# Kernel tuning notes

Measured on AMD Instinct MI355X. Metric: run time of the kernel, lower is better.

Reference implementation:

```python
import jax, jax.numpy as jnp
import numpy as np

H = 50  # hidden size
I = 1   # input size


def setup_inputs() -> dict:
    key = jax.random.key(0)
    ks = jax.random.split(key, 7)
    B, T = 4096, 512
    s = 1.0 / np.sqrt(H)  # PyTorch default init scale
    x = jax.random.normal(ks[0], (B, T, I), dtype=jnp.float32)
    W_ih = jax.random.uniform(ks[1], (4 * H, I), jnp.float32, -s, s)
    W_hh = jax.random.uniform(ks[2], (4 * H, H), jnp.float32, -s, s)
    b_ih = jax.random.uniform(ks[3], (4 * H,), jnp.float32, -s, s)
    b_hh = jax.random.uniform(ks[4], (4 * H,), jnp.float32, -s, s)
    W_out = jax.random.uniform(ks[5], (1, H), jnp.float32, -s, s)
    b_out = jax.random.uniform(ks[6], (1,), jnp.float32, -s, s)
    return {"x": x, "W_ih": W_ih, "W_hh": W_hh, "b_ih": b_ih,
            "b_hh": b_hh, "W_out": W_out, "b_out": b_out}


def _lstm(x, W_ih, W_hh, b_ih, b_hh):
    # x: [B, T, I]; gate order in PyTorch: i, f, g, o
    B = x.shape[0]
    b = b_ih + b_hh
    # precompute input projection for all timesteps: [T, B, 4H]
    xg = jnp.einsum('bti,gi->tbg', x, W_ih) + b

    def step(carry, xg_t):
        h, c = carry
        gates = xg_t + h @ W_hh.T  # [B, 4H]
        i, f, g, o = jnp.split(gates, 4, axis=-1)
        c = jax.nn.sigmoid(f) * c + jax.nn.sigmoid(i) * jnp.tanh(g)
        h = jax.nn.sigmoid(o) * jnp.tanh(c)
        return (h, c), h

    h0 = jnp.zeros((B, H), x.dtype)
    c0 = jnp.zeros((B, H), x.dtype)
    _, hs = jax.lax.scan(step, (h0, c0), xg)  # hs: [T, B, H]
    return hs.transpose(1, 0, 2)  # [B, T, H]


def reference(x, W_ih, W_hh, b_ih, b_hh, W_out, b_out):
    h = _lstm(x, W_ih, W_hh, b_ih, b_hh)          # [B, T, H]
    return h @ W_out.T + b_out                     # [B, T, 1]
```

## Files before the change

### kernel.cpp

```cpp
#include <hip/hip_runtime.h>
#include <math.h>

#define HID 50
#define TT  512
#define BT  16
#define NTH 448
#define HS  72
#define L2E 1.44269504088896f
#define K2C 2.88539008177793f

typedef __attribute__((ext_vector_type(8))) short bf16x8;
typedef __attribute__((ext_vector_type(4))) float f32x4;

__device__ __forceinline__ unsigned short bf16_rtne(float f) {
    unsigned u = __float_as_uint(f);
    u = (u + 0x7FFFu + ((u >> 16) & 1u)) >> 16;
    return (unsigned short)u;
}
__device__ __forceinline__ float bf16_f32(unsigned short s) {
    return __uint_as_float(((unsigned)s) << 16);
}

__global__ __launch_bounds__(NTH, 1) void lstm_mfma19_kernel(
    const float* __restrict__ x,
    const float* __restrict__ W_ih,
    const float* __restrict__ W_hh,
    const float* __restrict__ b_ih,
    const float* __restrict__ b_hh,
    const float* __restrict__ W_out,
    const float* __restrict__ b_out,
    float* __restrict__ out)
{
    const int tid  = threadIdx.x;
    const int lane = tid & 63;
    const int wv   = tid >> 6;
    const int col  = lane & 15;
    const int quad = lane >> 4;

    __shared__ __align__(16) unsigned short Hh[2][BT][HS];

    for (int i = tid; i < 2 * BT * HS; i += NTH)
        (&Hh[0][0][0])[i] = 0;

    bf16x8 Ah[2][2];
    float cs0 = 0.f, cs1 = 0.f;
    const int uoa = wv * 8 + quad;
    const int uob = wv * 8 + 4 + quad;
    const int uom = (quad == 1) ? 48 : (quad == 2) ? 49 : (quad == 0) ? 55 : 56;
    const int s0 = (wv < 6) ? uoa : uom;
    const int s1 = (wv < 6) ? uob : 57;

    if (wv < 6) {
        #pragma unroll
        for (int i = 0; i < 2; ++i) {
            const int gh  = (wv * 2 + i) * 16 + col;
            const int u   = gh >> 2;
            const int ty  = gh & 3;
            const int og  = ty * HID + u;
            const float sc = (ty == 2) ? K2C : L2E;
            #pragma unroll
            for (int kk = 0; kk < 2; ++kk) {
                #pragma unroll
                for (int j = 0; j < 8; ++j) {
                    const int k = kk * 32 + quad * 8 + j;
                    float v = 0.f;
                    if (k < HID)      v = sc * W_hh[og * HID + k];
                    else if (k == 50) v = sc * W_ih[og];
                    else if (k == 51) v = sc * (b_ih[og] + b_hh[og]);
                    else if (k == 52) v = sc * W_ih[og];
                    else if (k == 53) {
                        const float sb = sc * (b_ih[og] + b_hh[og]);
                        v = sb - bf16_f32(bf16_rtne(sb));
                    } else if (k == 54) {
                        const float sw = sc * W_ih[og];
                        v = sw - bf16_f32(bf16_rtne(sw));
                    }
                    Ah[i][kk][j] = (short)bf16_rtne(v);
                }
            }
        }
    } else {
        #pragma unroll
        for (int kk = 0; kk < 2; ++kk) {
            #pragma unroll
            for (int j = 0; j < 8; ++j) {
                const int k = kk * 32 + quad * 8 + j;
                float v = 0.f;
                if (col < 2) {
                    if (k < HID) {
                        const float w = W_out[k];
                        v = (col == 0) ? w : w - bf16_f32(bf16_rtne(w));
                    }
                } else if (col >= 4 && col < 12) {
                    const int u  = (col < 8) ? 48 : 49;
                    const int ty = col & 3;
                    const int og = ty * HID + u;
                    const float sc = (ty == 2) ? K2C : L2E;
                    if (k < HID)      v = sc * W_hh[og * HID + k];
                    else if (k == 50) v = sc * W_ih[og];
                    else if (k == 51) v = sc * (b_ih[og] + b_hh[og]);
                    else if (k == 52) v = sc * W_ih[og];
                    else if (k == 53) {
                        const float sb = sc * (b_ih[og] + b_hh[og]);
                        v = sb - bf16_f32(bf16_rtne(sb));
                    } else if (k == 54) {
                        const float sw = sc * W_ih[og];
                        v = sw - bf16_f32(bf16_rtne(sw));
                    }
                }
                Ah[0][kk][j] = (short)bf16_rtne(v);
                Ah[1][kk][j] = 0;
            }
        }
    }
    const float bo = b_out[0];
    float* yout = out + (size_t)blockIdx.x * BT * TT + (size_t)col * TT;

    const float* xrow = x + (size_t)(blockIdx.x * BT + col) * TT;
    float xa = 0.f;
    if (wv == 6 && lane >= 48)
        xa = xrow[1];

    __syncthreads();

    if (tid < BT) {
        const float x0 = x[(size_t)(blockIdx.x * BT + tid) * TT];
        const unsigned short hx = bf16_rtne(x0);
        const unsigned short lx = bf16_rtne(x0 - bf16_f32(hx));
        unsigned* row32 = (unsigned*)&Hh[0][tid][0];
        row32[25] = (unsigned)hx | (0x3F80u << 16);
        row32[26] = (unsigned)lx | (0x3F80u << 16);
        Hh[0][tid][54] = hx;
    }
    __syncthreads();

    const unsigned short* rdA = &Hh[0][col][quad * 8];
    const unsigned short* rdB = &Hh[1][col][quad * 8];
    unsigned short* wrA0 = &Hh[1][col][s0];
    unsigned short* wrA1 = &Hh[1][col][s1];
    unsigned short* wrB0 = &Hh[0][col][s0];
    unsigned short* wrB1 = &Hh[0][col][s1];
    unsigned* xwA = (unsigned*)&Hh[1][col][0];
    unsigned* xwB = (unsigned*)&Hh[0][col][0];
    const f32x4 z = {0.f, 0.f, 0.f, 0.f};

#define GATES(ACC, CS, HOUT)                                                  \
    do {                                                                      \
        const float Ei = __builtin_amdgcn_exp2f(-(ACC).x);                    \
        const float Ef = __builtin_amdgcn_exp2f(-(ACC).y);                    \
        const float Eg = __builtin_amdgcn_exp2f((ACC).z);                     \
        const float Eo = __builtin_amdgcn_exp2f(-(ACC).w);                    \
        const float DIG = (1.f + Ei) * (1.f + Eg);                            \
        const float DF  = 1.f + Ef;                                           \
        const float t1  = fmaf(K2C, Eg, -K2C);                                \
        const float num = fmaf((CS), DIG, t1 * DF);                           \
        (CS) = num * __builtin_amdgcn_rcpf(DF * DIG);                         \
        const float Ec = __builtin_amdgcn_exp2f(CS);                          \
        (HOUT) = (Ec - 1.f) *                                                 \
                 __builtin_amdgcn_rcpf((1.f + Eo) * (1.f + Ec));              \
    } while (0)

#define LSTM_STEP(RD, WR0, WR1, XW, TI)                                       \
    do {                                                                      \
        const bf16x8 B0 = *(const bf16x8*)(RD);                               \
        const bf16x8 B1 = *(const bf16x8*)((RD) + 32);                        \
        if (wv < 6) {                                                         \
            f32x4 a0 = __builtin_amdgcn_mfma_f32_16x16x32_bf16(Ah[0][0], B0, z, 0, 0, 0); \
            f32x4 a1 = __builtin_amdgcn_mfma_f32_16x16x32_bf16(Ah[1][0], B0, z, 0, 0, 0); \
            a0 = __builtin_amdgcn_mfma_f32_16x16x32_bf16(Ah[0][1], B1, a0, 0, 0, 0); \
            a1 = __builtin_amdgcn_mfma_f32_16x16x32_bf16(Ah[1][1], B1, a1, 0, 0, 0); \
            float h0, h1;                                                     \
            GATES(a0, cs0, h0);                                               \
            GATES(a1, cs1, h1);                                               \
            unsigned hpk;                                                     \
            asm("v_cvt_pk_bf16_f32 %0, %1, %2" : "=v"(hpk) : "v"(h0), "v"(h1)); \
            *(WR0) = (unsigned short)(hpk & 0xFFFFu);                         \
            *(WR1) = (unsigned short)(hpk >> 16);                             \
        } else {                                                              \
            if (lane >= 48) {                                                 \
                const unsigned short hx = bf16_rtne(xa);                      \
                const unsigned short lx = bf16_rtne(xa - bf16_f32(hx));       \
                (XW)[25] = (unsigned)hx | (0x3F80u << 16);                    \
                (XW)[26] = (unsigned)lx | (0x3F80u << 16);                    \
                ((unsigned short*)(XW))[54] = hx;                             \
                xa = xrow[((TI) + 2 < TT) ? (TI) + 2 : TT - 1];               \
            }                                                                 \
            f32x4 a0 = __builtin_amdgcn_mfma_f32_16x16x32_bf16(Ah[0][0], B0, z, 0, 0, 0); \
            a0 = __builtin_amdgcn_mfma_f32_16x16x32_bf16(Ah[0][1], B1, a0, 0, 0, 0); \
            float h0;                                                         \
            GATES(a0, cs0, h0);                                               \
            unsigned hpk;                                                     \
            asm("v_cvt_pk_bf16_f32 %0, %1, %2" : "=v"(hpk) : "v"(h0), "v"(h0)); \
            *(WR0) = (unsigned short)(hpk & 0xFFFFu);                         \
            if (lane < 16 && (TI) > 0)                                        \
                yout[(TI) - 1] = a0.x + a0.y + bo;                            \
        }                                                                     \
    } while (0)

    for (int t = 0; t < TT; t += 2) {
        LSTM_STEP(rdA, wrA0, wrA1, xwA, t);
        asm volatile("s_waitcnt lgkmcnt(0)\n\ts_barrier" ::: "memory");
        LSTM_STEP(rdB, wrB0, wrB1, xwB, t + 1);
        asm volatile("s_waitcnt lgkmcnt(0)\n\ts_barrier" ::: "memory");
    }
#undef LSTM_STEP
#undef GATES

    if (wv == 6) {
        const bf16x8 B0 = *(const bf16x8*)rdA;
        const bf16x8 B1 = *(const bf16x8*)(rdA + 32);
        f32x4 a0 = __builtin_amdgcn_mfma_f32_16x16x32_bf16(Ah[0][0], B0, z, 0, 0, 0);
        a0 = __builtin_amdgcn_mfma_f32_16x16x32_bf16(Ah[0][1], B1, a0, 0, 0, 0);
        if (lane < 16)
            yout[TT - 1] = a0.x + a0.y + bo;
    }
}

extern "C" void kernel_launch(void* const* d_in, const int* in_sizes, int n_in,
                              void* d_out, int out_size, void* d_ws, size_t ws_size,
                              hipStream_t stream) {
    const float* x     = (const float*)d_in[0];
    const float* W_ih  = (const float*)d_in[1];
    const float* W_hh  = (const float*)d_in[2];
    const float* b_ih  = (const float*)d_in[3];
    const float* b_hh  = (const float*)d_in[4];
    const float* W_out = (const float*)d_in[5];
    const float* b_out = (const float*)d_in[6];
    float* out = (float*)d_out;

    const int B = in_sizes[0] / TT;
    lstm_mfma19_kernel<<<B / BT, NTH, 0, stream>>>(x, W_ih, W_hh, b_ih, b_hh,
                                                   W_out, b_out, out);
}
```

Baseline: 245.6 us.

## Redistribute LSTM gate tiles across eight waves instead of seven

Raises the block from 7 to 8 waves and remaps the gate tiles. Waves 0-3 each compute two 16-gate tiles, wave 4 handles one tile plus the extra units 48/49 and the output projection, and waves 5-7 each compute one tile. Wave 5 also takes over staging the input x. Before, six waves carried two tiles each on the serial per-step critical path. With this layout only four waves run the dual-MFMA plus dual-gate path, which is meant to spread the per-step gate math more evenly and shorten the slowest wave before each barrier. The cost is one more wave joining every barrier, and wave 4 now does extra conditional gate work plus the output store.

```diff
diff --git a/kernel.cpp b/kernel.cpp
--- a/kernel.cpp
+++ b/kernel.cpp
@@ -4,7 +4,7 @@
 #define HID 50
 #define TT  512
 #define BT  16
-#define NTH 448
+#define NTH 512
 #define HS  72
 #define L2E 1.44269504088896f
 #define K2C 2.88539008177793f
@@ -21,7 +21,7 @@
     return __uint_as_float(((unsigned)s) << 16);
 }
 
-__global__ __launch_bounds__(NTH, 1) void lstm_mfma19_kernel(
+__global__ __launch_bounds__(NTH, 1) void lstm_mfma20_kernel(
     const float* __restrict__ x,
     const float* __restrict__ W_ih,
     const float* __restrict__ W_hh,
@@ -44,42 +44,43 @@
 
     bf16x8 Ah[2][2];
     float cs0 = 0.f, cs1 = 0.f;
-    const int uoa = wv * 8 + quad;
-    const int uob = wv * 8 + 4 + quad;
-    const int uom = (quad == 1) ? 48 : (quad == 2) ? 49 : (quad == 0) ? 55 : 56;
-    const int s0 = (wv < 6) ? uoa : uom;
-    const int s1 = (wv < 6) ? uob : 57;
-
-    if (wv < 6) {
-        #pragma unroll
-        for (int i = 0; i < 2; ++i) {
-            const int gh  = (wv * 2 + i) * 16 + col;
-            const int u   = gh >> 2;
-            const int ty  = gh & 3;
-            const int og  = ty * HID + u;
-            const float sc = (ty == 2) ? K2C : L2E;
-            #pragma unroll
-            for (int kk = 0; kk < 2; ++kk) {
-                #pragma unroll
-                for (int j = 0; j < 8; ++j) {
-                    const int k = kk * 32 + quad * 8 + j;
-                    float v = 0.f;
-                    if (k < HID)      v = sc * W_hh[og * HID + k];
-                    else if (k == 50) v = sc * W_ih[og];
-                    else if (k == 51) v = sc * (b_ih[og] + b_hh[og]);
-                    else if (k == 52) v = sc * W_ih[og];
-                    else if (k == 53) {
-                        const float sb = sc * (b_ih[og] + b_hh[og]);
-                        v = sb - bf16_f32(bf16_rtne(sb));
-                    } else if (k == 54) {
-                        const float sw = sc * W_ih[og];
-                        v = sw - bf16_f32(bf16_rtne(sw));
-                    }
-                    Ah[i][kk][j] = (short)bf16_rtne(v);
-                }
-            }
-        }
-    } else {
+    const int s0 = (wv < 4) ? wv * 8 + quad : wv * 4 + 16 + quad;
+    const int s1 = wv * 8 + 4 + quad;
+    const int sM = (quad == 1) ? 48 : 49;
+
+#define FILL_GATE_ROW(DST, GH)                                                \
+    do {                                                                      \
+        const int u_  = (GH) >> 2;                                            \
+        const int ty_ = (GH) & 3;                                             \
+        const int og_ = ty_ * HID + u_;                                       \
+        const float sc_ = (ty_ == 2) ? K2C : L2E;                             \
+        _Pragma("unroll")                                                     \
+        for (int kk = 0; kk < 2; ++kk) {                                      \
+            _Pragma("unroll")                                                 \
+            for (int j = 0; j < 8; ++j) {                                     \
+                const int k = kk * 32 + quad * 8 + j;                         \
+                float v = 0.f;                                                \
+                if (k < HID)      v = sc_ * W_hh[og_ * HID + k];              \
+                else if (k == 50) v = sc_ * W_ih[og_];                        \
+                else if (k == 51) v = sc_ * (b_ih[og_] + b_hh[og_]);          \
+                else if (k == 52) v = sc_ * W_ih[og_];                        \
+                else if (k == 53) {                                           \
+                    const float sb = sc_ * (b_ih[og_] + b_hh[og_]);           \
+                    v = sb - bf16_f32(bf16_rtne(sb));                         \
+                } else if (k == 54) {                                         \
+                    const float sw = sc_ * W_ih[og_];                         \
+                    v = sw - bf16_f32(bf16_rtne(sw));                         \
+                }                                                             \
+                (DST)[kk][j] = (short)bf16_rtne(v);                           \
+            }                                                                 \
+        }                                                                     \
+    } while (0)
+
+    if (wv < 4) {
+        FILL_GATE_ROW(Ah[0], (wv * 2) * 16 + col);
+        FILL_GATE_ROW(Ah[1], (wv * 2 + 1) * 16 + col);
+    } else if (wv == 4) {
+        FILL_GATE_ROW(Ah[0], 8 * 16 + col);
         #pragma unroll
         for (int kk = 0; kk < 2; ++kk) {
             #pragma unroll
@@ -92,33 +93,40 @@
                         v = (col == 0) ? w : w - bf16_f32(bf16_rtne(w));
                     }
                 } else if (col >= 4 && col < 12) {
-                    const int u  = (col < 8) ? 48 : 49;
-                    const int ty = col & 3;
-                    const int og = ty * HID + u;
-                    const float sc = (ty == 2) ? K2C : L2E;
-                    if (k < HID)      v = sc * W_hh[og * HID + k];
-                    else if (k == 50) v = sc * W_ih[og];
-                    else if (k == 51) v = sc * (b_ih[og] + b_hh[og]);
-                    else if (k == 52) v = sc * W_ih[og];
+                    const int u_  = (col < 8) ? 48 : 49;
+                    const int ty_ = col & 3;
+                    const int og_ = ty_ * HID + u_;
+                    const float sc_ = (ty_ == 2) ? K2C : L2E;
+                    if (k < HID)      v = sc_ * W_hh[og_ * HID + k];
+                    else if (k == 50) v = sc_ * W_ih[og_];
+                    else if (k == 51) v = sc_ * (b_ih[og_] + b_hh[og_]);
+                    else if (k == 52) v = sc_ * W_ih[og_];
                     else if (k == 53) {
-                        const float sb = sc * (b_ih[og] + b_hh[og]);
+                        const float sb = sc_ * (b_ih[og_] + b_hh[og_]);
                         v = sb - bf16_f32(bf16_rtne(sb));
                     } else if (k == 54) {
-                        const float sw = sc * W_ih[og];
+                        const float sw = sc_ * W_ih[og_];
                         v = sw - bf16_f32(bf16_rtne(sw));
                     }
                 }
-                Ah[0][kk][j] = (short)bf16_rtne(v);
-                Ah[1][kk][j] = 0;
+                Ah[1][kk][j] = (short)bf16_rtne(v);
             }
         }
-    }
+    } else {
+        FILL_GATE_ROW(Ah[0], (wv + 4) * 16 + col);
+        #pragma unroll
+        for (int kk = 0; kk < 2; ++kk)
+            #pragma unroll
+            for (int j = 0; j < 8; ++j) Ah[1][kk][j] = 0;
+    }
+#undef FILL_GATE_ROW
+
     const float bo = b_out[0];
     float* yout = out + (size_t)blockIdx.x * BT * TT + (size_t)col * TT;
 
     const float* xrow = x + (size_t)(blockIdx.x * BT + col) * TT;
     float xa = 0.f;
-    if (wv == 6 && lane >= 48)
+    if (wv == 5 && lane >= 48)
         xa = xrow[1];
 
     __syncthreads();
@@ -138,8 +146,10 @@
     const unsigned short* rdB = &Hh[1][col][quad * 8];
     unsigned short* wrA0 = &Hh[1][col][s0];
     unsigned short* wrA1 = &Hh[1][col][s1];
+    unsigned short* wrAM = &Hh[1][col][sM];
     unsigned short* wrB0 = &Hh[0][col][s0];
     unsigned short* wrB1 = &Hh[0][col][s1];
+    unsigned short* wrBM = &Hh[0][col][sM];
     unsigned* xwA = (unsigned*)&Hh[1][col][0];
     unsigned* xwB = (unsigned*)&Hh[0][col][0];
     const f32x4 z = {0.f, 0.f, 0.f, 0.f};
@@ -160,11 +170,11 @@
                  __builtin_amdgcn_rcpf((1.f + Eo) * (1.f + Ec));              \
     } while (0)
 
-#define LSTM_STEP(RD, WR0, WR1, XW, TI)                                       \
+#define LSTM_STEP(RD, WR0, WR1, WRM, XW, TI)                                  \
     do {                                                                      \
         const bf16x8 B0 = *(const bf16x8*)(RD);                               \
         const bf16x8 B1 = *(const bf16x8*)((RD) + 32);                        \
-        if (wv < 6) {                                                         \
+        if (wv < 4) {                                                         \
             f32x4 a0 = __builtin_amdgcn_mfma_f32_16x16x32_bf16(Ah[0][0], B0, z, 0, 0, 0); \
             f32x4 a1 = __builtin_amdgcn_mfma_f32_16x16x32_bf16(Ah[1][0], B0, z, 0, 0, 0); \
             a0 = __builtin_amdgcn_mfma_f32_16x16x32_bf16(Ah[0][1], B1, a0, 0, 0, 0); \
@@ -176,8 +186,27 @@
             asm("v_cvt_pk_bf16_f32 %0, %1, %2" : "=v"(hpk) : "v"(h0), "v"(h1)); \
             *(WR0) = (unsigned short)(hpk & 0xFFFFu);                         \
             *(WR1) = (unsigned short)(hpk >> 16);                             \
+        } else if (wv == 4) {                                                 \
+            f32x4 a0 = __builtin_amdgcn_mfma_f32_16x16x32_bf16(Ah[0][0], B0, z, 0, 0, 0); \
+            f32x4 a1 = __builtin_amdgcn_mfma_f32_16x16x32_bf16(Ah[1][0], B0, z, 0, 0, 0); \
+            a0 = __builtin_amdgcn_mfma_f32_16x16x32_bf16(Ah[0][1], B1, a0, 0, 0, 0); \
+            a1 = __builtin_amdgcn_mfma_f32_16x16x32_bf16(Ah[1][1], B1, a1, 0, 0, 0); \
+            float h0;                                                         \
+            GATES(a0, cs0, h0);                                               \
+            unsigned hpk;                                                     \
+            asm("v_cvt_pk_bf16_f32 %0, %1, %2" : "=v"(hpk) : "v"(h0), "v"(h0)); \
+            *(WR0) = (unsigned short)(hpk & 0xFFFFu);                         \
+            if (quad == 1 || quad == 2) {      \
+                float h1;                                                     \
+                GATES(a1, cs1, h1);                                           \
+                unsigned hpm;                                                 \
+                asm("v_cvt_pk_bf16_f32 %0, %1, %2" : "=v"(hpm) : "v"(h1), "v"(h1)); \
+                *(WRM) = (unsigned short)(hpm & 0xFFFFu);                     \
+            }                                                                 \
+            if (lane < 16 && (TI) > 0)                                        \
+                yout[(TI) - 1] = a1.x + a1.y + bo;                            \
         } else {                                                              \
-            if (lane >= 48) {                                                 \
+            if (wv == 5 && lane >= 48) {                                      \
                 const unsigned short hx = bf16_rtne(xa);                      \
                 const unsigned short lx = bf16_rtne(xa - bf16_f32(hx));       \
                 (XW)[25] = (unsigned)hx | (0x3F80u << 16);                    \
@@ -192,27 +221,25 @@
             unsigned hpk;                                                     \
             asm("v_cvt_pk_bf16_f32 %0, %1, %2" : "=v"(hpk) : "v"(h0), "v"(h0)); \
             *(WR0) = (unsigned short)(hpk & 0xFFFFu);                         \
-            if (lane < 16 && (TI) > 0)                                        \
-                yout[(TI) - 1] = a0.x + a0.y + bo;                            \
         }                                                                     \
     } while (0)
 
     for (int t = 0; t < TT; t += 2) {
-        LSTM_STEP(rdA, wrA0, wrA1, xwA, t);
+        LSTM_STEP(rdA, wrA0, wrA1, wrAM, xwA, t);
         asm volatile("s_waitcnt lgkmcnt(0)\n\ts_barrier" ::: "memory");
-        LSTM_STEP(rdB, wrB0, wrB1, xwB, t + 1);
+        LSTM_STEP(rdB, wrB0, wrB1, wrBM, xwB, t + 1);
         asm volatile("s_waitcnt lgkmcnt(0)\n\ts_barrier" ::: "memory");
     }
 #undef LSTM_STEP
 #undef GATES
 
-    if (wv == 6) {
+    if (wv == 4) {
         const bf16x8 B0 = *(const bf16x8*)rdA;
         const bf16x8 B1 = *(const bf16x8*)(rdA + 32);
-        f32x4 a0 = __builtin_amdgcn_mfma_f32_16x16x32_bf16(Ah[0][0], B0, z, 0, 0, 0);
-        a0 = __builtin_amdgcn_mfma_f32_16x16x32_bf16(Ah[0][1], B1, a0, 0, 0, 0);
+        f32x4 a1 = __builtin_amdgcn_mfma_f32_16x16x32_bf16(Ah[1][0], B0, z, 0, 0, 0);
+        a1 = __builtin_amdgcn_mfma_f32_16x16x32_bf16(Ah[1][1], B1, a1, 0, 0, 0);
         if (lane < 16)
-            yout[TT - 1] = a0.x + a0.y + bo;
+            yout[TT - 1] = a1.x + a1.y + bo;
     }
 }
 
@@ -229,6 +256,6 @@
     float* out = (float*)d_out;
 
     const int B = in_sizes[0] / TT;
-    lstm_mfma19_kernel<<<B / BT, NTH, 0, stream>>>(x, W_ih, W_hh, b_ih, b_hh,
+    lstm_mfma20_kernel<<<B / BT, NTH, 0, stream>>>(x, W_ih, W_hh, b_ih, b_hh,
                                                    W_out, b_out, out);
 }
```

Measured after the change: 253.8 us. 3.3% more time.
